# Performance work log

Measured on AMD Instinct MI355X. Metric: run time of the kernel, lower is better.

The kernel has to match this reference:

```python
import jax, jax.numpy as jnp
import numpy as np

B, C, N, S = 16, 128, 32768, 100


def setup_inputs() -> dict:
    key = jax.random.key(0)
    k1, k2 = jax.random.split(key)
    point_features = jax.random.normal(k1, (B, C, N), dtype=jnp.float32)
    cluster_ids = jax.random.randint(k2, (B, N), 0, S, dtype=jnp.int32)
    return {"point_features": point_features, "cluster_ids": cluster_ids, "num_segments": S}


def reference(point_features, cluster_ids, num_segments):
    # point_features: (B, C, N); cluster_ids: (B, N) int labels in [0, num_segments)
    # Original: for each pc, for each segment label, boolean-mask points and
    # max-pool over the point axis -> per-(pc, segment) max over channels.
    # Fused equivalent: per-batch segment_max over the point axis.
    feats = jnp.transpose(point_features, (0, 2, 1))  # (B, N, C)
    seg_max = jax.vmap(
        lambda f, l: jax.ops.segment_max(f, l, num_segments=num_segments)
    )(feats, cluster_ids)  # (B, S, C)
    # vstack over all (pc, segment) pairs -> (B*S, C)
    return seg_max.reshape(-1, seg_max.shape[-1])
```

## Files before the change

### kernel.cpp

```cpp
#include <hip/hip_runtime.h>

#define Bc 16
#define Cc 128
#define Nc 32768
#define Sc 100
#define CHUNK 1024
#define BLOCK 256
#define SPAD 129
#define MONO_NEG_INF 0x007FFFFFu

__device__ __forceinline__ unsigned enc(float f) {
    unsigned u = __float_as_uint(f);
    unsigned m = (unsigned)((int)u >> 31);
    return u ^ (m | 0x80000000u);
}
__device__ __forceinline__ float dec(unsigned v) {
    unsigned m = ~(unsigned)((int)v >> 31);
    return __uint_as_float(v ^ (m | 0x80000000u));
}

__global__ void init_kernel(unsigned* __restrict__ out_u, int n) {
    int i = blockIdx.x * blockDim.x + threadIdx.x;
    if (i < n) out_u[i] = MONO_NEG_INF;
}

__global__ __launch_bounds__(BLOCK) void seg_max_kernel(
        const float* __restrict__ pf, const int* __restrict__ ids,
        unsigned* __restrict__ out_u) {
    __shared__ unsigned acc[Sc * SPAD];
    const int tid = threadIdx.x;
    const int chunk = blockIdx.x;
    const int b = blockIdx.y;
    const int n0 = chunk * CHUNK;

    for (int i = tid; i < Sc * SPAD; i += BLOCK) acc[i] = MONO_NEG_INF;

    const int4 id4 = reinterpret_cast<const int4*>(ids + (size_t)b * Nc + n0)[tid];
    const int o0 = id4.x * SPAD;
    const int o1 = id4.y * SPAD;
    const int o2 = id4.z * SPAD;
    const int o3 = id4.w * SPAD;

    __syncthreads();

    const float* base = pf + (size_t)b * Cc * Nc + n0;
    #pragma unroll 4
    for (int c = 0; c < Cc; ++c) {
        float4 v = reinterpret_cast<const float4*>(base + (size_t)c * Nc)[tid];
        atomicMax(&acc[o0 + c], enc(v.x));
        atomicMax(&acc[o1 + c], enc(v.y));
        atomicMax(&acc[o2 + c], enc(v.z));
        atomicMax(&acc[o3 + c], enc(v.w));
    }

    __syncthreads();

    unsigned* out_b = out_u + (size_t)b * Sc * Cc;
    for (int i = tid; i < Sc * Cc; i += BLOCK) {
        int s = i >> 7, c = i & 127;
        unsigned v = acc[s * SPAD + c];
        if (v != MONO_NEG_INF) atomicMax(&out_b[i], v);
    }
}

__global__ void convert_kernel(unsigned* __restrict__ out_u, int n) {
    int i = blockIdx.x * blockDim.x + threadIdx.x;
    if (i < n) {
        float f = dec(out_u[i]);
        reinterpret_cast<float*>(out_u)[i] = f;
    }
}

extern "C" void kernel_launch(void* const* d_in, const int* in_sizes, int n_in,
                              void* d_out, int out_size, void* d_ws, size_t ws_size,
                              hipStream_t stream) {
    const float* pf = (const float*)d_in[0];
    const int* ids = (const int*)d_in[1];
    unsigned* out_u = (unsigned*)d_out;

    const int n = Bc * Sc * Cc;
    init_kernel<<<(n + 255) / 256, 256, 0, stream>>>(out_u, n);

    dim3 grid(Nc / CHUNK, Bc);
    seg_max_kernel<<<grid, BLOCK, 0, stream>>>(pf, ids, out_u);

    convert_kernel<<<(n + 255) / 256, 256, 0, stream>>>(out_u, n);
}
```

Measured before the change: 382.9 us.

## Replace global atomic merge with per-chunk partials and a separate reduce kernel

Each block now writes its full shared-memory segment/channel max table to a workspace slice instead of issuing global atomicMax into the output. A second kernel reduces the 32 partials per batch with vectorized loads and decodes straight to float, so the init and convert kernels are no longer needed. The main-loop unroll also goes from 4 to 8. This removes global atomic contention and one launch, but adds about 26 MB of workspace writes and reads and depends on the workspace being large enough.

```diff
diff --git a/kernel.cpp b/kernel.cpp
--- a/kernel.cpp
+++ b/kernel.cpp
@@ -4,9 +4,11 @@
 #define Cc 128
 #define Nc 32768
 #define Sc 100
+#define NCHUNK 32
 #define CHUNK 1024
 #define BLOCK 256
 #define SPAD 129
+#define PART (Sc * Cc)
 #define MONO_NEG_INF 0x007FFFFFu
 
 __device__ __forceinline__ unsigned enc(float f) {
@@ -19,14 +21,9 @@
     return __uint_as_float(v ^ (m | 0x80000000u));
 }
 
-__global__ void init_kernel(unsigned* __restrict__ out_u, int n) {
-    int i = blockIdx.x * blockDim.x + threadIdx.x;
-    if (i < n) out_u[i] = MONO_NEG_INF;
-}
-
-__global__ __launch_bounds__(BLOCK) void seg_max_kernel(
+__global__ __launch_bounds__(BLOCK) void seg_part_kernel(
         const float* __restrict__ pf, const int* __restrict__ ids,
-        unsigned* __restrict__ out_u) {
+        unsigned* __restrict__ parts) {
     __shared__ unsigned acc[Sc * SPAD];
     const int tid = threadIdx.x;
     const int chunk = blockIdx.x;
@@ -44,7 +41,7 @@
     __syncthreads();
 
     const float* base = pf + (size_t)b * Cc * Nc + n0;
-    #pragma unroll 4
+    #pragma unroll 8
     for (int c = 0; c < Cc; ++c) {
         float4 v = reinterpret_cast<const float4*>(base + (size_t)c * Nc)[tid];
         atomicMax(&acc[o0 + c], enc(v.x));
@@ -55,20 +52,31 @@
 
     __syncthreads();
 
-    unsigned* out_b = out_u + (size_t)b * Sc * Cc;
-    for (int i = tid; i < Sc * Cc; i += BLOCK) {
-        int s = i >> 7, c = i & 127;
-        unsigned v = acc[s * SPAD + c];
-        if (v != MONO_NEG_INF) atomicMax(&out_b[i], v);
-    }
+    unsigned* dst = parts + (size_t)(b * NCHUNK + chunk) * PART;
+    for (int i = tid; i < PART; i += BLOCK)
+        dst[i] = acc[(i >> 7) * SPAD + (i & 127)];
 }
 
-__global__ void convert_kernel(unsigned* __restrict__ out_u, int n) {
-    int i = blockIdx.x * blockDim.x + threadIdx.x;
-    if (i < n) {
-        float f = dec(out_u[i]);
-        reinterpret_cast<float*>(out_u)[i] = f;
+__global__ __launch_bounds__(BLOCK) void seg_reduce_kernel(
+        const unsigned* __restrict__ parts, float* __restrict__ out) {
+    const int t = blockIdx.x * BLOCK + threadIdx.x;
+    const int e0 = t * 4;
+    const int b = e0 / PART;
+    const int r = e0 % PART;
+
+    const unsigned* p = parts + (size_t)b * NCHUNK * PART + r;
+    unsigned mx = MONO_NEG_INF, my = MONO_NEG_INF,
+             mz = MONO_NEG_INF, mw = MONO_NEG_INF;
+    #pragma unroll
+    for (int k = 0; k < NCHUNK; ++k) {
+        uint4 v = *reinterpret_cast<const uint4*>(p + (size_t)k * PART);
+        mx = v.x > mx ? v.x : mx;
+        my = v.y > my ? v.y : my;
+        mz = v.z > mz ? v.z : mz;
+        mw = v.w > mw ? v.w : mw;
     }
+    float4 o = { dec(mx), dec(my), dec(mz), dec(mw) };
+    *reinterpret_cast<float4*>(out + e0) = o;
 }
 
 extern "C" void kernel_launch(void* const* d_in, const int* in_sizes, int n_in,
@@ -76,13 +84,12 @@
                               hipStream_t stream) {
     const float* pf = (const float*)d_in[0];
     const int* ids = (const int*)d_in[1];
-    unsigned* out_u = (unsigned*)d_out;
+    float* out = (float*)d_out;
+    unsigned* parts = (unsigned*)d_ws;
 
-    const int n = Bc * Sc * Cc;
-    init_kernel<<<(n + 255) / 256, 256, 0, stream>>>(out_u, n);
+    dim3 gridA(NCHUNK, Bc);
+    seg_part_kernel<<<gridA, BLOCK, 0, stream>>>(pf, ids, parts);
 
-    dim3 grid(Nc / CHUNK, Bc);
-    seg_max_kernel<<<grid, BLOCK, 0, stream>>>(pf, ids, out_u);
-
-    convert_kernel<<<(n + 255) / 256, 256, 0, stream>>>(out_u, n);
+    const int n = Bc * PART;
+    seg_reduce_kernel<<<(n / 4) / BLOCK, BLOCK, 0, stream>>>(parts, out);
 }
```

Measured after the change: 379.5 us. No clear change (-0.9%).
